# Kernel tuning notes

Measured on AMD Instinct MI355X. Metric: run time of the kernel, lower is better.

## Reference

```python
import jax, jax.numpy as jnp
import numpy as np

N_NODES = 100000
N_EDGES = 800000
EPS = 1e-5


def _mean_agg(h, src, dst):
    # DGL SAGEConv 'mean': average of in-neighbor features per dst node.
    msg = jnp.take(h, src, axis=0)                      # [E, D] gather
    summed = jax.ops.segment_sum(msg, dst, num_segments=N_NODES)
    deg = jax.ops.segment_sum(jnp.ones((src.shape[0],), h.dtype), dst,
                              num_segments=N_NODES)
    return summed / jnp.maximum(deg, 1.0)[:, None]


def _sage(h, src, dst, ws, wn, b):
    # rst = fc_self(h) + fc_neigh(mean_neigh) + bias
    return h @ ws + _mean_agg(h, src, dst) @ wn + b


def _bn(x, g, b, m, v):
    return (x - m) * (g / jnp.sqrt(v + EPS)) + b


def setup_inputs() -> dict:
    key = jax.random.key(0)
    ks = jax.random.split(key, 16)
    s = 0.02
    inp = {
        "structural_features": jax.random.normal(ks[0], (N_NODES, 128), jnp.float32),
        "multimodal_features": jax.random.normal(ks[1], (N_NODES, 384), jnp.float32),
        "src": jax.random.randint(ks[2], (N_EDGES,), 0, N_NODES),
        "dst": jax.random.randint(ks[3], (N_EDGES,), 0, N_NODES),
        "enc_w": jax.random.normal(ks[4], (512, 128), jnp.float32) * s,
        "enc_b": jnp.zeros((128,), jnp.float32),
        "sage0_ws": jax.random.normal(ks[5], (128, 256), jnp.float32) * s,
        "sage0_wn": jax.random.normal(ks[6], (128, 256), jnp.float32) * s,
        "sage0_b": jnp.zeros((256,), jnp.float32),
        "bn0_g": jnp.ones((256,), jnp.float32),
        "bn0_b": jnp.zeros((256,), jnp.float32),
        "bn0_m": jnp.zeros((256,), jnp.float32),
        "bn0_v": jnp.ones((256,), jnp.float32),
        "sage1_ws": jax.random.normal(ks[7], (256, 128), jnp.float32) * s,
        "sage1_wn": jax.random.normal(ks[8], (256, 128), jnp.float32) * s,
        "sage1_b": jnp.zeros((128,), jnp.float32),
        "bn1_g": jnp.ones((128,), jnp.float32),
        "bn1_b": jnp.zeros((128,), jnp.float32),
        "bn1_m": jnp.zeros((128,), jnp.float32),
        "bn1_v": jnp.ones((128,), jnp.float32),
        "rel_w": jax.random.normal(ks[9], (256, 128), jnp.float32) * s,
        "rel_b": jnp.zeros((128,), jnp.float32),
        "cls_w1": jax.random.normal(ks[10], (128, 64), jnp.float32) * s,
        "cls_b1": jnp.zeros((64,), jnp.float32),
        "cls_w2": jax.random.normal(ks[11], (64, 32), jnp.float32) * s,
        "cls_b2": jnp.zeros((32,), jnp.float32),
    }
    return inp


def reference(structural_features, multimodal_features, src, dst,
              enc_w, enc_b,
              sage0_ws, sage0_wn, sage0_b, bn0_g, bn0_b, bn0_m, bn0_v,
              sage1_ws, sage1_wn, sage1_b, bn1_g, bn1_b, bn1_m, bn1_v,
              rel_w, rel_b, cls_w1, cls_b1, cls_w2, cls_b2):
    x = jnp.concatenate([structural_features, multimodal_features], axis=-1)
    h0 = jax.nn.relu(x @ enc_w + enc_b)                     # input_encoder (dropout=eval)
    h = jax.nn.relu(_bn(_sage(h0, src, dst, sage0_ws, sage0_wn, sage0_b),
                        bn0_g, bn0_b, bn0_m, bn0_v))
    h = jax.nn.relu(_bn(_sage(h, src, dst, sage1_ws, sage1_wn, sage1_b),
                        bn1_g, bn1_b, bn1_m, bn1_v))
    h_final = jnp.concatenate([h0, h], axis=1)              # [N, 256]
    h_final = jax.nn.relu(h_final @ rel_w + rel_b)          # relation_encoder
    out = jax.nn.relu(h_final @ cls_w1 + cls_b1) @ cls_w2 + cls_b2
    return out
```

## Files before the change

kernel.cpp:

```cpp
#include <hip/hip_runtime.h>
#include <math.h>


#define EPS 1e-5f

typedef __attribute__((ext_vector_type(8))) short bf16x8;
typedef __attribute__((ext_vector_type(4))) float f32x4;

__device__ inline unsigned short f2bf(float x) {
    unsigned u = __float_as_uint(x);
    u += 0x7fff + ((u >> 16) & 1);
    return (unsigned short)(u >> 16);
}
__device__ inline float bf2f(unsigned short h) {
    return __uint_as_float(((unsigned)h) << 16);
}
__device__ inline unsigned packbf(float x, float y) {
    return (unsigned)f2bf(x) | ((unsigned)f2bf(y) << 16);
}

__device__ inline void gload_lds16(const void* g, void* l) {
    __builtin_amdgcn_global_load_lds(
        (__attribute__((address_space(1))) void*)g,
        (__attribute__((address_space(3))) void*)l, 16, 0, 0);
}


__global__ void zero_int(int* __restrict__ p, int n) {
    int i = blockIdx.x * 256 + threadIdx.x;
    if (i < n) p[i] = 0;
}

__global__ void count_deg(const int* __restrict__ dst, int* __restrict__ deg, int e) {
    int i = blockIdx.x * 256 + threadIdx.x;
    if (i < e) atomicAdd(&deg[dst[i]], 1);
}

__global__ __launch_bounds__(1024)
void scan_block(const int* __restrict__ deg, int* __restrict__ rowptr,
                int* __restrict__ part, int n) {
    __shared__ int buf[1024];
    const int tid = threadIdx.x;
    const int i = blockIdx.x * 1024 + tid;
    const int v = (i < n) ? deg[i] : 0;
    buf[tid] = v;
    __syncthreads();
    #pragma unroll 1
    for (int off = 1; off < 1024; off <<= 1) {
        int t = (tid >= off) ? buf[tid - off] : 0;
        __syncthreads();
        buf[tid] += t;
        __syncthreads();
    }
    if (i < n) rowptr[i] = buf[tid] - v;
    if (tid == 1023) part[blockIdx.x] = buf[1023];
}

__global__ __launch_bounds__(1024)
void scan_part(int* __restrict__ part, int nb) {
    __shared__ int buf[1024];
    const int tid = threadIdx.x;
    const int v = (tid < nb) ? part[tid] : 0;
    buf[tid] = v;
    __syncthreads();
    #pragma unroll 1
    for (int off = 1; off < 1024; off <<= 1) {
        int t = (tid >= off) ? buf[tid - off] : 0;
        __syncthreads();
        buf[tid] += t;
        __syncthreads();
    }
    if (tid < nb) part[tid] = buf[tid] - v;
    if (tid == 1023) part[nb] = buf[1023];
}

__global__ void scan_add(const int* __restrict__ part, int* __restrict__ rowptr,
                         int* __restrict__ cursor, int n, int nb) {
    int i = blockIdx.x * 256 + threadIdx.x;
    if (i < n) {
        int v = rowptr[i] + part[i >> 10];
        rowptr[i] = v;
        cursor[i] = v;
    }
    if (i == 0) rowptr[n] = part[nb];
}

__global__ void fill_edges(const int* __restrict__ src, const int* __restrict__ dst,
                           int* __restrict__ cursor, int* __restrict__ eidx, int e) {
    int i = blockIdx.x * 256 + threadIdx.x;
    if (i < e) {
        int pos = atomicAdd(&cursor[dst[i]], 1);
        eidx[pos] = src[i];
    }
}


__global__ void prep_w(const float* __restrict__ W, int K, int N,
                       short* __restrict__ hi, short* __restrict__ lo,
                       int ldt, int koff) {
    int i = blockIdx.x * 256 + threadIdx.x;
    if (i >= K * N) return;
    int k = i / N, n = i - k * N;
    float x = W[i];
    unsigned short h = f2bf(x);
    unsigned short l = f2bf(x - bf2f(h));
    size_t o = (size_t)n * ldt + koff + k;
    hi[o] = (short)h;
    lo[o] = (short)l;
}


__global__ __launch_bounds__(256)
void concat_bf16(const float* __restrict__ sf, const float* __restrict__ mf,
                 short* __restrict__ xb, int nn) {
    const int total = nn * 64;
    for (int g = blockIdx.x * 256 + threadIdx.x; g < total; g += gridDim.x * 256) {
        const int n = g >> 6, u = g & 63;
        const float* p = (u < 16) ? (sf + (size_t)n * 128 + (size_t)u * 8)
                                  : (mf + (size_t)n * 384 + (size_t)(u - 16) * 8);
        const float4 f0 = ((const float4*)p)[0];
        const float4 f1 = ((const float4*)p)[1];
        uint4 o;
        o.x = packbf(f0.x, f0.y); o.y = packbf(f0.z, f0.w);
        o.z = packbf(f1.x, f1.y); o.w = packbf(f1.z, f1.w);
        *(uint4*)(xb + (size_t)g * 8) = o;
    }
}


__global__ __launch_bounds__(256)
void agg_mean_bb(const short* __restrict__ featb,
                 const int* __restrict__ rowptr, const int* __restrict__ eidx,
                 short* __restrict__ outb, int n) {
    const int node = blockIdx.x * 4 + (threadIdx.x >> 6);
    if (node >= n) return;
    const int lane = threadIdx.x & 63;
    const int g = lane >> 4, j = lane & 15;
    const int beg = rowptr[node], end = rowptr[node + 1];
    float s[8];
    #pragma unroll
    for (int i = 0; i < 8; ++i) s[i] = 0.f;
    for (int e = beg + g; e < end; e += 4) {
        const uint4 v = *(const uint4*)(featb + (size_t)eidx[e] * 128 + j * 8);
        s[0] += __uint_as_float(v.x << 16); s[1] += __uint_as_float(v.x & 0xffff0000u);
        s[2] += __uint_as_float(v.y << 16); s[3] += __uint_as_float(v.y & 0xffff0000u);
        s[4] += __uint_as_float(v.z << 16); s[5] += __uint_as_float(v.z & 0xffff0000u);
        s[6] += __uint_as_float(v.w << 16); s[7] += __uint_as_float(v.w & 0xffff0000u);
    }
    #pragma unroll
    for (int i = 0; i < 8; ++i) {
        s[i] += __shfl_xor(s[i], 32);
        s[i] += __shfl_xor(s[i], 16);
    }
    if (g == 0) {
        const float inv = 1.0f / fmaxf((float)(end - beg), 1.0f);
        uint4 o;
        o.x = packbf(s[0] * inv, s[1] * inv);
        o.y = packbf(s[2] * inv, s[3] * inv);
        o.z = packbf(s[4] * inv, s[5] * inv);
        o.w = packbf(s[6] * inv, s[7] * inv);
        *(uint4*)(outb + (size_t)node * 128 + j * 8) = o;
    }
}

__global__ __launch_bounds__(256)
void agg_combine_bb(const short* __restrict__ featb,
                    const int* __restrict__ rowptr, const int* __restrict__ eidx,
                    const float* __restrict__ s1,
                    const float* __restrict__ bias,
                    const float* __restrict__ bng, const float* __restrict__ bnb,
                    const float* __restrict__ bnm, const float* __restrict__ bnv,
                    short* __restrict__ outb, int n) {
    const int node = blockIdx.x * 4 + (threadIdx.x >> 6);
    if (node >= n) return;
    const int lane = threadIdx.x & 63;
    const int g = lane >> 4, j = lane & 15;
    const int beg = rowptr[node], end = rowptr[node + 1];
    float s[8];
    #pragma unroll
    for (int i = 0; i < 8; ++i) s[i] = 0.f;
    for (int e = beg + g; e < end; e += 4) {
        const uint4 v = *(const uint4*)(featb + (size_t)eidx[e] * 128 + j * 8);
        s[0] += __uint_as_float(v.x << 16); s[1] += __uint_as_float(v.x & 0xffff0000u);
        s[2] += __uint_as_float(v.y << 16); s[3] += __uint_as_float(v.y & 0xffff0000u);
        s[4] += __uint_as_float(v.z << 16); s[5] += __uint_as_float(v.z & 0xffff0000u);
        s[6] += __uint_as_float(v.w << 16); s[7] += __uint_as_float(v.w & 0xffff0000u);
    }
    #pragma unroll
    for (int i = 0; i < 8; ++i) {
        s[i] += __shfl_xor(s[i], 32);
        s[i] += __shfl_xor(s[i], 16);
    }
    if (g == 0) {
        const float inv = 1.0f / fmaxf((float)(end - beg), 1.0f);
        const int c0 = j * 8;
        const float4 a0 = *(const float4*)(s1 + (size_t)node * 128 + c0);
        const float4 a1 = *(const float4*)(s1 + (size_t)node * 128 + c0 + 4);
        const float sf[8] = {a0.x, a0.y, a0.z, a0.w, a1.x, a1.y, a1.z, a1.w};
        float r[8];
        #pragma unroll
        for (int i = 0; i < 8; ++i) {
            const int c = c0 + i;
            float v = sf[i] + s[i] * inv + bias[c];
            v = (v - bnm[c]) * (bng[c] / sqrtf(bnv[c] + EPS)) + bnb[c];
            r[i] = fmaxf(v, 0.f);
        }
        uint4 o;
        o.x = packbf(r[0], r[1]); o.y = packbf(r[2], r[3]);
        o.z = packbf(r[4], r[5]); o.w = packbf(r[6], r[7]);
        *(uint4*)(outb + (size_t)node * 128 + j * 8) = o;
    }
}

template<int NT, int K1, int K2>
__global__ __launch_bounds__(256)
void gemm_dp(const short* __restrict__ A1, int lda1,
             const short* __restrict__ A2, int lda2,
             const short* __restrict__ Wt_hi, const short* __restrict__ Wt_lo,
             const float* __restrict__ bias,
             const float* __restrict__ bng, const float* __restrict__ bnb,
             const float* __restrict__ bnm, const float* __restrict__ bnv,
             int relu,
             float* __restrict__ Cf, int fpN, int ldc,
             short* __restrict__ Cb, int bfcol0, int ldcb,
             int M) {
    constexpr int K   = K1 + K2;
    constexpr int NBK = K / 64;
    static_assert(K % 64 == 0, "K multiple of 64");
    static_assert(K2 == 0 || K1 % 64 == 0, "concat boundary on BK");
    constexpr int ASZ = 128 * 64;
    constexpr int BSZ = 2 * NT * 16 * 64;
    constexpr int BUF = ASZ + BSZ;
    __shared__ short lds[2 * BUF];

    const int tid  = threadIdx.x;
    const int lane = tid & 63;
    const int wv   = tid >> 6;
    const int bm   = blockIdx.y * 128;
    const int col0 = blockIdx.x * (NT * 16);
    const int lrow = lane & 15;
    const int quad = lane >> 4;

    const int su = (tid & 7) ^ ((tid >> 3) & 7);
    const short* gsA1[4];
    const short* gsA2[4];
    #pragma unroll
    for (int jj = 0; jj < 4; ++jj) {
        const int rg = min(bm + jj * 32 + (tid >> 3), M - 1);
        gsA1[jj] = A1 + (size_t)rg * lda1 + su * 8;
        if constexpr (K2 > 0) gsA2[jj] = A2 + (size_t)rg * lda2 + su * 8;
        else gsA2[jj] = nullptr;
    }
    const short* gsB[NT];
    #pragma unroll
    for (int jj = 0; jj < NT; ++jj) {
        const int colIdx = jj * 32 + (tid >> 3);
        const bool ishi = colIdx < NT * 16;
        const int cp = ishi ? colIdx : colIdx - NT * 16;
        gsB[jj] = (ishi ? Wt_hi : Wt_lo) + (size_t)(col0 + cp) * K + su * 8;
    }

    auto stage = [&](int b, int c) {
        const int k = c * 64;
        #pragma unroll
        for (int jj = 0; jj < 4; ++jj) {
            const short* p;
            if constexpr (K2 > 0)
                p = (k < K1) ? (gsA1[jj] + k) : (gsA2[jj] + (k - K1));
            else
                p = gsA1[jj] + k;
            gload_lds16(p, &lds[b * BUF + (jj * 256 + tid) * 8]);
        }
        #pragma unroll
        for (int jj = 0; jj < NT; ++jj)
            gload_lds16(gsB[jj] + k, &lds[b * BUF + ASZ + (jj * 256 + tid) * 8]);
    };

    int aoff[2][2];
    #pragma unroll
    for (int m = 0; m < 2; ++m)
        #pragma unroll
        for (int kk = 0; kk < 2; ++kk)
            aoff[m][kk] = (wv * 32 + m * 16 + lrow) * 64 +
                          (((kk * 4 + quad) ^ (lrow & 7)) * 8);
    int boff[NT][2];
    #pragma unroll
    for (int nt = 0; nt < NT; ++nt)
        #pragma unroll
        for (int kk = 0; kk < 2; ++kk)
            boff[nt][kk] = (nt * 16 + lrow) * 64 +
                           (((kk * 4 + quad) ^ (lrow & 7)) * 8);

    f32x4 acc[2][NT];
    #pragma unroll
    for (int m = 0; m < 2; ++m)
        #pragma unroll
        for (int nt = 0; nt < NT; ++nt)
            acc[m][nt] = (f32x4){0.f, 0.f, 0.f, 0.f};

    stage(0, 0);

    for (int c = 0; c < NBK; ++c) {
        const int b = c & 1;
        if (c + 1 < NBK) {
            stage(b ^ 1, c + 1);
            if constexpr (NT == 4) asm volatile("s_waitcnt vmcnt(8)" ::: "memory");
            else                   asm volatile("s_waitcnt vmcnt(6)" ::: "memory");
        } else {
            asm volatile("s_waitcnt vmcnt(0)" ::: "memory");
        }
        __builtin_amdgcn_s_barrier();

        const short* La = &lds[b * BUF];
        const short* Lb = &lds[b * BUF + ASZ];
        #pragma unroll
        for (int kk = 0; kk < 2; ++kk) {
            const bf16x8 a0 = *(const bf16x8*)(La + aoff[0][kk]);
            const bf16x8 a1 = *(const bf16x8*)(La + aoff[1][kk]);
            #pragma unroll
            for (int nt = 0; nt < NT; ++nt) {
                const bf16x8 vbh = *(const bf16x8*)(Lb + boff[nt][kk]);
                const bf16x8 vbl = *(const bf16x8*)(Lb + boff[nt][kk] + NT * 16 * 64);
                acc[0][nt] = __builtin_amdgcn_mfma_f32_16x16x32_bf16(a0, vbh, acc[0][nt], 0, 0, 0);
                acc[0][nt] = __builtin_amdgcn_mfma_f32_16x16x32_bf16(a0, vbl, acc[0][nt], 0, 0, 0);
                acc[1][nt] = __builtin_amdgcn_mfma_f32_16x16x32_bf16(a1, vbh, acc[1][nt], 0, 0, 0);
                acc[1][nt] = __builtin_amdgcn_mfma_f32_16x16x32_bf16(a1, vbl, acc[1][nt], 0, 0, 0);
            }
        }
        asm volatile("" ::: "memory");
        __builtin_amdgcn_s_barrier();
    }

    constexpr int EW = NT * 16 + 4;
    float* ep = (float*)lds;

    #pragma unroll
    for (int nt = 0; nt < NT; ++nt) {
        const int gcol = col0 + nt * 16 + lrow;
        const float bsc = bias ? bias[gcol] : 0.f;
        float gg = 1.f, bb = 0.f, mm = 0.f;
        if (bng) { gg = bng[gcol] / sqrtf(bnv[gcol] + EPS); bb = bnb[gcol]; mm = bnm[gcol]; }
        #pragma unroll
        for (int m = 0; m < 2; ++m) {
            #pragma unroll
            for (int r = 0; r < 4; ++r) {
                float x = acc[m][nt][r] + bsc;
                if (bng) x = (x - mm) * gg + bb;
                if (relu) x = fmaxf(x, 0.f);
                ep[(wv * 32 + m * 16 + quad * 4 + r) * EW + nt * 16 + lrow] = x;
            }
        }
    }
    __syncthreads();

    if (col0 < fpN) {
        for (int g = tid; g < 128 * NT * 4; g += 256) {
            const int row = g / (NT * 4), u = g - row * (NT * 4);
            const int grow = bm + row;
            if (grow < M)
                *(float4*)(Cf + (size_t)grow * ldc + col0 + u * 4) =
                    *(const float4*)(ep + row * EW + u * 4);
        }
    } else {
        for (int g = tid; g < 128 * NT * 2; g += 256) {
            const int row = g / (NT * 2), u = g - row * (NT * 2);
            const int grow = bm + row;
            const float4 f0 = *(const float4*)(ep + row * EW + u * 8);
            const float4 f1 = *(const float4*)(ep + row * EW + u * 8 + 4);
            uint4 o;
            o.x = packbf(f0.x, f0.y); o.y = packbf(f0.z, f0.w);
            o.z = packbf(f1.x, f1.y); o.w = packbf(f1.z, f1.w);
            if (grow < M)
                *(uint4*)(Cb + (size_t)grow * ldcb + (col0 - bfcol0) + u * 8) = o;
        }
    }
}


extern "C" void kernel_launch(void* const* d_in, const int* in_sizes, int n_in,
                              void* d_out, int out_size, void* d_ws, size_t ws_size,
                              hipStream_t stream) {
    const float* sf    = (const float*)d_in[0];
    const float* mf    = (const float*)d_in[1];
    const int*   src   = (const int*)d_in[2];
    const int*   dst   = (const int*)d_in[3];
    const float* enc_w = (const float*)d_in[4];
    const float* enc_b = (const float*)d_in[5];
    const float* s0_ws = (const float*)d_in[6];
    const float* s0_wn = (const float*)d_in[7];
    const float* s0_b  = (const float*)d_in[8];
    const float* bn0_g = (const float*)d_in[9];
    const float* bn0_b = (const float*)d_in[10];
    const float* bn0_m = (const float*)d_in[11];
    const float* bn0_v = (const float*)d_in[12];
    const float* s1_ws = (const float*)d_in[13];
    const float* s1_wn = (const float*)d_in[14];
    const float* s1_b  = (const float*)d_in[15];
    const float* bn1_g = (const float*)d_in[16];
    const float* bn1_b = (const float*)d_in[17];
    const float* bn1_m = (const float*)d_in[18];
    const float* bn1_v = (const float*)d_in[19];
    const float* rel_w = (const float*)d_in[20];
    const float* rel_b = (const float*)d_in[21];
    const float* cw1   = (const float*)d_in[22];
    const float* cb1   = (const float*)d_in[23];
    const float* cw2   = (const float*)d_in[24];
    const float* cb2   = (const float*)d_in[25];
    float* out = (float*)d_out;

    const int nn = in_sizes[0] / 128;
    const int ne = in_sizes[2];
    const int nb = (nn + 1023) / 1024;

    short* h0b   = (short*)d_ws;
    short* xb    = h0b + (size_t)nn * 128;
    float* st    = (float*)xb;
    short* h1b   = (short*)(st + (size_t)nn * 128);
    short* agg0b = xb + (size_t)nn * 512;
    short* t1b   = agg0b + (size_t)nn * 128;
    short* h2b   = t1b + (size_t)nn * 128;
    short* o1b   = agg0b;
    short* rb    = t1b;
    int* deg    = (int*)(h2b + (size_t)nn * 128);
    int* rowptr = deg + nn;
    int* cursor = rowptr + nn + 1;
    int* part   = cursor + nn;
    int* eidx   = part + nb + 1;
    short* wts = (short*)(eidx + ne);
    short* wt_enc_h = wts;                 short* wt_enc_l = wt_enc_h + 65536;
    short* wt_s0_h  = wt_enc_l + 65536;    short* wt_s0_l  = wt_s0_h  + 65536;
    short* wt_st_h  = wt_s0_l  + 65536;    short* wt_st_l  = wt_st_h  + 65536;
    short* wt_rel_h = wt_st_l  + 65536;    short* wt_rel_l = wt_rel_h + 32768;
    short* wt_c1_h  = wt_rel_l + 32768;    short* wt_c1_l  = wt_c1_h  + 8192;
    short* wt_c2_h  = wt_c1_l  + 8192;     short* wt_c2_l  = wt_c2_h  + 2048;

    const dim3 blk(256);
    const int gM = (nn + 127) / 128;

    zero_int  <<<dim3((nn + 255) / 256), blk, 0, stream>>>(deg, nn);
    count_deg <<<dim3((ne + 255) / 256), blk, 0, stream>>>(dst, deg, ne);
    scan_block<<<dim3(nb), dim3(1024), 0, stream>>>(deg, rowptr, part, nn);
    scan_part <<<dim3(1),  dim3(1024), 0, stream>>>(part, nb);
    scan_add  <<<dim3((nn + 255) / 256), blk, 0, stream>>>(part, rowptr, cursor, nn, nb);
    fill_edges<<<dim3((ne + 255) / 256), blk, 0, stream>>>(src, dst, cursor, eidx, ne);

    prep_w<<<dim3(256), blk, 0, stream>>>(enc_w, 512, 128, wt_enc_h, wt_enc_l, 512, 0);
    prep_w<<<dim3(128), blk, 0, stream>>>(s0_ws, 128, 256, wt_s0_h, wt_s0_l, 256, 0);
    prep_w<<<dim3(128), blk, 0, stream>>>(s0_wn, 128, 256, wt_s0_h, wt_s0_l, 256, 128);
    prep_w<<<dim3(128), blk, 0, stream>>>(s1_ws, 256, 128, wt_st_h, wt_st_l, 256, 0);
    prep_w<<<dim3(128), blk, 0, stream>>>(s1_wn, 256, 128, wt_st_h + (size_t)128 * 256,
                                          wt_st_l + (size_t)128 * 256, 256, 0);
    prep_w<<<dim3(128), blk, 0, stream>>>(rel_w, 256, 128, wt_rel_h, wt_rel_l, 256, 0);
    prep_w<<<dim3(32),  blk, 0, stream>>>(cw1, 128, 64, wt_c1_h, wt_c1_l, 128, 0);
    prep_w<<<dim3(8),   blk, 0, stream>>>(cw2, 64, 32, wt_c2_h, wt_c2_l, 64, 0);

    concat_bf16<<<dim3(2048), blk, 0, stream>>>(sf, mf, xb, nn);

    gemm_dp<4, 512, 0><<<dim3(2, gM), blk, 0, stream>>>(
        xb, 512, nullptr, 0, wt_enc_h, wt_enc_l, enc_b,
        nullptr, nullptr, nullptr, nullptr, 1,
        nullptr, 0, 0, h0b, 0, 128, nn);

    agg_mean_bb<<<dim3((nn + 3) / 4), blk, 0, stream>>>(
        h0b, rowptr, eidx, agg0b, nn);

    gemm_dp<4, 128, 128><<<dim3(4, gM), blk, 0, stream>>>(
        h0b, 128, agg0b, 128, wt_s0_h, wt_s0_l, s0_b,
        bn0_g, bn0_b, bn0_m, bn0_v, 1,
        nullptr, 0, 0, h1b, 0, 256, nn);

    gemm_dp<4, 256, 0><<<dim3(4, gM), blk, 0, stream>>>(
        h1b, 256, nullptr, 0, wt_st_h, wt_st_l, nullptr,
        nullptr, nullptr, nullptr, nullptr, 0,
        st, 128, 128, t1b, 128, 128, nn);

    agg_combine_bb<<<dim3((nn + 3) / 4), blk, 0, stream>>>(
        t1b, rowptr, eidx, st, s1_b,
        bn1_g, bn1_b, bn1_m, bn1_v, h2b, nn);

    gemm_dp<4, 128, 128><<<dim3(2, gM), blk, 0, stream>>>(
        h0b, 128, h2b, 128, wt_rel_h, wt_rel_l, rel_b,
        nullptr, nullptr, nullptr, nullptr, 1,
        nullptr, 0, 0, rb, 0, 128, nn);

    gemm_dp<4, 128, 0><<<dim3(1, gM), blk, 0, stream>>>(
        rb, 128, nullptr, 0, wt_c1_h, wt_c1_l, cb1,
        nullptr, nullptr, nullptr, nullptr, 1,
        nullptr, 0, 0, o1b, 0, 64, nn);

    gemm_dp<2, 64, 0><<<dim3(1, gM), blk, 0, stream>>>(
        o1b, 64, nullptr, 0, wt_c2_h, wt_c2_l, cb2,
        nullptr, nullptr, nullptr, nullptr, 0,
        out, 32, 32, nullptr, 0, 0, nn);
}
```

Baseline: 718.8 us.

## Merge weight-prep launches, batch concat loads, and retile GEMM warps 2x2

Folds the eight per-weight split-precision conversion kernels into one launch. Replaces the zeroing kernel with a memset. Changes the concat/bf16 conversion to issue four independent row loads per thread before storing. Reorganizes the GEMM wave layout from 4x1 to 2x2 so each wave reuses B fragments across four M subtiles, trading fewer LDS reads for more accumulator registers.

```diff
diff --git a/kernel.cpp b/kernel.cpp
--- a/kernel.cpp
+++ b/kernel.cpp
@@ -25,11 +25,6 @@
         (__attribute__((address_space(3))) void*)l, 16, 0, 0);
 }
 
-
-__global__ void zero_int(int* __restrict__ p, int n) {
-    int i = blockIdx.x * 256 + threadIdx.x;
-    if (i < n) p[i] = 0;
-}
 
 __global__ void count_deg(const int* __restrict__ dst, int* __restrict__ deg, int e) {
     int i = blockIdx.x * 256 + threadIdx.x;
@@ -95,16 +90,30 @@
 }
 
 
-__global__ void prep_w(const float* __restrict__ W, int K, int N,
-                       short* __restrict__ hi, short* __restrict__ lo,
-                       int ldt, int koff) {
-    int i = blockIdx.x * 256 + threadIdx.x;
-    if (i >= K * N) return;
-    int k = i / N, n = i - k * N;
-    float x = W[i];
-    unsigned short h = f2bf(x);
-    unsigned short l = f2bf(x - bf2f(h));
-    size_t o = (size_t)n * ldt + koff + k;
+__global__ __launch_bounds__(256)
+void prep_all(const float* __restrict__ enc_w, const float* __restrict__ s0_ws,
+              const float* __restrict__ s0_wn, const float* __restrict__ s1_ws,
+              const float* __restrict__ s1_wn, const float* __restrict__ rel_w,
+              const float* __restrict__ cw1, const float* __restrict__ cw2,
+              short* wt_enc_h, short* wt_enc_l, short* wt_s0_h, short* wt_s0_l,
+              short* wt_st_h, short* wt_st_l, short* wt_rel_h, short* wt_rel_l,
+              short* wt_c1_h, short* wt_c1_l, short* wt_c2_h, short* wt_c2_l) {
+    int e = blockIdx.x * 256 + threadIdx.x;
+    const float* W; short* hi; short* lo; int Nd, ldt, koff;
+    if (e < 65536)       { W = enc_w; hi = wt_enc_h; lo = wt_enc_l; Nd = 128; ldt = 512; koff = 0; }
+    else if (e < 98304)  { e -= 65536;  W = s0_ws; hi = wt_s0_h; lo = wt_s0_l; Nd = 256; ldt = 256; koff = 0; }
+    else if (e < 131072) { e -= 98304;  W = s0_wn; hi = wt_s0_h; lo = wt_s0_l; Nd = 256; ldt = 256; koff = 128; }
+    else if (e < 163840) { e -= 131072; W = s1_ws; hi = wt_st_h; lo = wt_st_l; Nd = 128; ldt = 256; koff = 0; }
+    else if (e < 196608) { e -= 163840; W = s1_wn; hi = wt_st_h + 32768; lo = wt_st_l + 32768; Nd = 128; ldt = 256; koff = 0; }
+    else if (e < 229376) { e -= 196608; W = rel_w; hi = wt_rel_h; lo = wt_rel_l; Nd = 128; ldt = 256; koff = 0; }
+    else if (e < 237568) { e -= 229376; W = cw1; hi = wt_c1_h; lo = wt_c1_l; Nd = 64; ldt = 128; koff = 0; }
+    else if (e < 239616) { e -= 237568; W = cw2; hi = wt_c2_h; lo = wt_c2_l; Nd = 32; ldt = 64; koff = 0; }
+    else return;
+    const int k = e / Nd, n = e - k * Nd;
+    const float x = W[e];
+    const unsigned short h = f2bf(x);
+    const unsigned short l = f2bf(x - bf2f(h));
+    const size_t o = (size_t)n * ldt + koff + k;
     hi[o] = (short)h;
     lo[o] = (short)l;
 }
@@ -113,17 +122,25 @@
 __global__ __launch_bounds__(256)
 void concat_bf16(const float* __restrict__ sf, const float* __restrict__ mf,
                  short* __restrict__ xb, int nn) {
-    const int total = nn * 64;
-    for (int g = blockIdx.x * 256 + threadIdx.x; g < total; g += gridDim.x * 256) {
-        const int n = g >> 6, u = g & 63;
-        const float* p = (u < 16) ? (sf + (size_t)n * 128 + (size_t)u * 8)
-                                  : (mf + (size_t)n * 384 + (size_t)(u - 16) * 8);
-        const float4 f0 = ((const float4*)p)[0];
-        const float4 f1 = ((const float4*)p)[1];
+    const int S = nn * 16;
+    const int g = blockIdx.x * 256 + threadIdx.x;
+    if (g >= S) return;
+    const int q = g & 63;
+    float4 f[4][2];
+    #pragma unroll
+    for (int j = 0; j < 4; ++j) {
+        const int n = (g + j * S) >> 6;
+        const float* p = (q < 16) ? (sf + (size_t)n * 128 + (size_t)q * 8)
+                                  : (mf + (size_t)n * 384 + (size_t)(q - 16) * 8);
+        f[j][0] = ((const float4*)p)[0];
+        f[j][1] = ((const float4*)p)[1];
+    }
+    #pragma unroll
+    for (int j = 0; j < 4; ++j) {
         uint4 o;
-        o.x = packbf(f0.x, f0.y); o.y = packbf(f0.z, f0.w);
-        o.z = packbf(f1.x, f1.y); o.w = packbf(f1.z, f1.w);
-        *(uint4*)(xb + (size_t)g * 8) = o;
+        o.x = packbf(f[j][0].x, f[j][0].y); o.y = packbf(f[j][0].z, f[j][0].w);
+        o.z = packbf(f[j][1].x, f[j][1].y); o.w = packbf(f[j][1].z, f[j][1].w);
+        *(uint4*)(xb + (size_t)(g + j * S) * 8) = o;
     }
 }
 
@@ -226,7 +243,9 @@
              int M) {
     constexpr int K   = K1 + K2;
     constexpr int NBK = K / 64;
+    constexpr int NTW = NT / 2;
     static_assert(K % 64 == 0, "K multiple of 64");
+    static_assert(NT % 2 == 0, "NT even");
     static_assert(K2 == 0 || K1 % 64 == 0, "concat boundary on BK");
     constexpr int ASZ = 128 * 64;
     constexpr int BSZ = 2 * NT * 16 * 64;
@@ -236,6 +255,8 @@
     const int tid  = threadIdx.x;
     const int lane = tid & 63;
     const int wv   = tid >> 6;
+    const int wm   = wv >> 1;
+    const int wn   = wv & 1;
     const int bm   = blockIdx.y * 128;
     const int col0 = blockIdx.x * (NT * 16);
     const int lrow = lane & 15;
@@ -276,26 +297,26 @@
             gload_lds16(gsB[jj] + k, &lds[b * BUF + ASZ + (jj * 256 + tid) * 8]);
     };
 
-    int aoff[2][2];
-    #pragma unroll
-    for (int m = 0; m < 2; ++m)
+    int aoff[4][2];
+    #pragma unroll
+    for (int m = 0; m < 4; ++m)
         #pragma unroll
         for (int kk = 0; kk < 2; ++kk)
-            aoff[m][kk] = (wv * 32 + m * 16 + lrow) * 64 +
+            aoff[m][kk] = (wm * 64 + m * 16 + lrow) * 64 +
                           (((kk * 4 + quad) ^ (lrow & 7)) * 8);
-    int boff[NT][2];
-    #pragma unroll
-    for (int nt = 0; nt < NT; ++nt)
+    int boff[NTW][2];
+    #pragma unroll
+    for (int nt = 0; nt < NTW; ++nt)
         #pragma unroll
         for (int kk = 0; kk < 2; ++kk)
-            boff[nt][kk] = (nt * 16 + lrow) * 64 +
+            boff[nt][kk] = (wn * NTW * 16 + nt * 16 + lrow) * 64 +
                            (((kk * 4 + quad) ^ (lrow & 7)) * 8);
 
-    f32x4 acc[2][NT];
-    #pragma unroll
-    for (int m = 0; m < 2; ++m)
-        #pragma unroll
-        for (int nt = 0; nt < NT; ++nt)
+    f32x4 acc[4][NTW];
+    #pragma unroll
+    for (int m = 0; m < 4; ++m)
+        #pragma unroll
+        for (int nt = 0; nt < NTW; ++nt)
             acc[m][nt] = (f32x4){0.f, 0.f, 0.f, 0.f};
 
     stage(0, 0);
@@ -315,16 +336,19 @@
         const short* Lb = &lds[b * BUF + ASZ];
         #pragma unroll
         for (int kk = 0; kk < 2; ++kk) {
-            const bf16x8 a0 = *(const bf16x8*)(La + aoff[0][kk]);
-            const bf16x8 a1 = *(const bf16x8*)(La + aoff[1][kk]);
+            bf16x8 a[4];
             #pragma unroll
-            for (int nt = 0; nt < NT; ++nt) {
+            for (int m = 0; m < 4; ++m)
+                a[m] = *(const bf16x8*)(La + aoff[m][kk]);
+            #pragma unroll
+            for (int nt = 0; nt < NTW; ++nt) {
                 const bf16x8 vbh = *(const bf16x8*)(Lb + boff[nt][kk]);
                 const bf16x8 vbl = *(const bf16x8*)(Lb + boff[nt][kk] + NT * 16 * 64);
-                acc[0][nt] = __builtin_amdgcn_mfma_f32_16x16x32_bf16(a0, vbh, acc[0][nt], 0, 0, 0);
-                acc[0][nt] = __builtin_amdgcn_mfma_f32_16x16x32_bf16(a0, vbl, acc[0][nt], 0, 0, 0);
-                acc[1][nt] = __builtin_amdgcn_mfma_f32_16x16x32_bf16(a1, vbh, acc[1][nt], 0, 0, 0);
-                acc[1][nt] = __builtin_amdgcn_mfma_f32_16x16x32_bf16(a1, vbl, acc[1][nt], 0, 0, 0);
+                #pragma unroll
+                for (int m = 0; m < 4; ++m) {
+                    acc[m][nt] = __builtin_amdgcn_mfma_f32_16x16x32_bf16(a[m], vbh, acc[m][nt], 0, 0, 0);
+                    acc[m][nt] = __builtin_amdgcn_mfma_f32_16x16x32_bf16(a[m], vbl, acc[m][nt], 0, 0, 0);
+                }
             }
         }
         asm volatile("" ::: "memory");
@@ -335,19 +359,20 @@
     float* ep = (float*)lds;
 
     #pragma unroll
-    for (int nt = 0; nt < NT; ++nt) {
-        const int gcol = col0 + nt * 16 + lrow;
+    for (int nt = 0; nt < NTW; ++nt) {
+        const int lcol = wn * NTW * 16 + nt * 16 + lrow;
+        const int gcol = col0 + lcol;
         const float bsc = bias ? bias[gcol] : 0.f;
         float gg = 1.f, bb = 0.f, mm = 0.f;
         if (bng) { gg = bng[gcol] / sqrtf(bnv[gcol] + EPS); bb = bnb[gcol]; mm = bnm[gcol]; }
         #pragma unroll
-        for (int m = 0; m < 2; ++m) {
+        for (int m = 0; m < 4; ++m) {
             #pragma unroll
             for (int r = 0; r < 4; ++r) {
                 float x = acc[m][nt][r] + bsc;
                 if (bng) x = (x - mm) * gg + bb;
                 if (relu) x = fmaxf(x, 0.f);
-                ep[(wv * 32 + m * 16 + quad * 4 + r) * EW + nt * 16 + lrow] = x;
+                ep[(wm * 64 + m * 16 + quad * 4 + r) * EW + lcol] = x;
             }
         }
     }
@@ -437,24 +462,19 @@
     const dim3 blk(256);
     const int gM = (nn + 127) / 128;
 
-    zero_int  <<<dim3((nn + 255) / 256), blk, 0, stream>>>(deg, nn);
+    hipMemsetAsync(deg, 0, (size_t)nn * 4, stream);
     count_deg <<<dim3((ne + 255) / 256), blk, 0, stream>>>(dst, deg, ne);
     scan_block<<<dim3(nb), dim3(1024), 0, stream>>>(deg, rowptr, part, nn);
     scan_part <<<dim3(1),  dim3(1024), 0, stream>>>(part, nb);
     scan_add  <<<dim3((nn + 255) / 256), blk, 0, stream>>>(part, rowptr, cursor, nn, nb);
     fill_edges<<<dim3((ne + 255) / 256), blk, 0, stream>>>(src, dst, cursor, eidx, ne);
 
-    prep_w<<<dim3(256), blk, 0, stream>>>(enc_w, 512, 128, wt_enc_h, wt_enc_l, 512, 0);
-    prep_w<<<dim3(128), blk, 0, stream>>>(s0_ws, 128, 256, wt_s0_h, wt_s0_l, 256, 0);
-    prep_w<<<dim3(128), blk, 0, stream>>>(s0_wn, 128, 256, wt_s0_h, wt_s0_l, 256, 128);
-    prep_w<<<dim3(128), blk, 0, stream>>>(s1_ws, 256, 128, wt_st_h, wt_st_l, 256, 0);
-    prep_w<<<dim3(128), blk, 0, stream>>>(s1_wn, 256, 128, wt_st_h + (size_t)128 * 256,
-                                          wt_st_l + (size_t)128 * 256, 256, 0);
-    prep_w<<<dim3(128), blk, 0, stream>>>(rel_w, 256, 128, wt_rel_h, wt_rel_l, 256, 0);
-    prep_w<<<dim3(32),  blk, 0, stream>>>(cw1, 128, 64, wt_c1_h, wt_c1_l, 128, 0);
-    prep_w<<<dim3(8),   blk, 0, stream>>>(cw2, 64, 32, wt_c2_h, wt_c2_l, 64, 0);
-
-    concat_bf16<<<dim3(2048), blk, 0, stream>>>(sf, mf, xb, nn);
+    prep_all<<<dim3(936), blk, 0, stream>>>(
+        enc_w, s0_ws, s0_wn, s1_ws, s1_wn, rel_w, cw1, cw2,
+        wt_enc_h, wt_enc_l, wt_s0_h, wt_s0_l, wt_st_h, wt_st_l,
+        wt_rel_h, wt_rel_l, wt_c1_h, wt_c1_l, wt_c2_h, wt_c2_l);
+
+    concat_bf16<<<dim3((nn * 16 + 255) / 256), blk, 0, stream>>>(sf, mf, xb, nn);
 
     gemm_dp<4, 512, 0><<<dim3(2, gM), blk, 0, stream>>>(
         xb, 512, nullptr, 0, wt_enc_h, wt_enc_l, enc_b,
```

New measurement: 699.2 us. 1.03x faster.
